# Performance work log

Hardware: AMD Instinct MI355X
Metric: run time of the kernel (lower is better)

## Reference

```python
import jax, jax.numpy as jnp
import numpy as np

N, D, H, E, K = 8192, 512, 2048, 8, 2  # tokens, input/output dim, hidden, experts, top-k
EPS = float(np.finfo(np.float64).eps)   # np.finfo(float).eps used by SparseDispatcher
NOISE_EPS = 1e-2                        # standard noisy-top-k gating epsilon


def setup_inputs() -> dict:
    key = jax.random.key(0)
    ks = jax.random.split(key, 8)
    s = 0.02  # weight scale to keep exp() in combine numerically sane
    return {
        "x": jax.random.normal(ks[0], (N, D), jnp.float32),
        "gate_feat": jax.random.normal(ks[1], (N, 2 * D), jnp.float32),
        "noise": jax.random.normal(ks[2], (N, E), jnp.float32),
        "w_gate": jax.random.normal(ks[3], (2 * D, E), jnp.float32) * s,
        "w_noise": jax.random.normal(ks[4], (2 * D, E), jnp.float32) * s,
        "fc1_w": jax.random.normal(ks[5], (E, H, D), jnp.float32) * s,
        "fc1_b": jnp.zeros((E, H), jnp.float32),
        "fc2_w": jax.random.normal(ks[6], (E, D, H), jnp.float32) * s,
        "fc2_b": jnp.zeros((E, D), jnp.float32),
    }


def reference(x, gate_feat, noise, w_gate, w_noise, fc1_w, fc1_b, fc2_w, fc2_b):
    # --- noisy top-k gating ---
    clean_logits = gate_feat @ w_gate                               # [N, E]
    noise_stddev = jax.nn.softplus(gate_feat @ w_noise) + NOISE_EPS  # [N, E]
    logits = clean_logits + noise * noise_stddev                    # randn_like * stddev
    top_vals, top_idx = jax.lax.top_k(logits, K + 1)                # top k+1 as in Shazeer gating
    top_k_gates = jax.nn.softmax(top_vals[:, :K], axis=-1)          # softmax over top-k logits
    gates = jnp.zeros_like(logits).at[jnp.arange(N)[:, None], top_idx[:, :K]].set(top_k_gates)

    # --- per-expert MLP (grouped GEMM; dense-masked form, math-equal to sparse dispatch
    # since zero-gate contributions vanish in the weighted combine) ---
    h = jax.nn.gelu(jnp.einsum('nd,ehd->enh', x, fc1_w) + fc1_b[:, None, :],
                    approximate=False)                              # torch nn.GELU = exact erf
    expert_out = jnp.einsum('enh,eoh->eno', h, fc2_w) + fc2_b[:, None, :]  # [E, N, D]

    # --- SparseDispatcher.combine: exp, gate-weight, scatter-add, eps-fill, log ---
    combined = jnp.einsum('ne,eno->no', gates, jnp.exp(expert_out))  # [N, D]
    combined = jnp.where(combined == 0, EPS, combined)
    return jnp.log(combined)
```

## Files before the change

### kernel.cpp

```cpp
#include <hip/hip_runtime.h>
#include <hip/hip_bf16.h>

#define NTOK 8192
#define DIM  512
#define HID  2048
#define NEXP 8
#define GFD  1024
#define NPAIR (NTOK*2)
#define EPSD 2.220446049250313e-16f
#define MAXTILES 136

typedef __bf16 bf16;
typedef __bf16 bf16x4 __attribute__((ext_vector_type(4)));
typedef __bf16 bf16x8 __attribute__((ext_vector_type(8)));
typedef float  f32x4  __attribute__((ext_vector_type(4)));

__device__ __forceinline__ void cvt4(const float* __restrict__ src,
                                     bf16* __restrict__ dst, int i) {
    float4 v = ((const float4*)src)[i];
    bf16x4 o = { (bf16)v.x, (bf16)v.y, (bf16)v.z, (bf16)v.w };
    ((bf16x4*)dst)[i] = o;
}

__global__ __launch_bounds__(256) void convert_kernel(
    const float* __restrict__ x, const float* __restrict__ w1,
    const float* __restrict__ w2,
    bf16* __restrict__ xo, bf16* __restrict__ w1o, bf16* __restrict__ w2o)
{
    int tid = blockIdx.x * 256 + threadIdx.x;
    int stride = gridDim.x * 256;
    for (int i = tid; i < NTOK*DIM/4; i += stride)      cvt4(x,  xo,  i);
    for (int i = tid; i < NEXP*HID*DIM/4; i += stride)  cvt4(w1, w1o, i);
    for (int i = tid; i < NEXP*DIM*HID/4; i += stride)  cvt4(w2, w2o, i);
}

__global__ __launch_bounds__(256) void gate_gemm_kernel(
    const float* __restrict__ gf, const float* __restrict__ wg,
    const float* __restrict__ wn, float* __restrict__ partial)
{
    const int bt = blockIdx.x;
    const int bd = blockIdx.y;
    const int tid = threadIdx.x;

    __shared__ float sgf[128*129];
    __shared__ float sw[128][16];

    #pragma unroll
    for (int i = 0; i < 4; ++i) {
        int idx = i*256 + tid;
        sw[idx>>3][idx&7]     = wg[bd*1024 + idx];
        sw[idx>>3][8+(idx&7)] = wn[bd*1024 + idx];
    }
    const float4* gf4 = (const float4*)gf;
    #pragma unroll
    for (int i = 0; i < 16; ++i) {
        int c = i*256 + tid;
        int row = c >> 5, c4 = c & 31;
        float4 v = gf4[(size_t)(bt*128+row)*(GFD/4) + bd*32 + c4];
        float* dst = sgf + row*129 + c4*4;
        dst[0]=v.x; dst[1]=v.y; dst[2]=v.z; dst[3]=v.w;
    }
    __syncthreads();

    const int og = tid >> 6;
    const int lane = tid & 63;
    const int t0 = lane*2, t1 = t0+1;
    float a0=0,a1=0,a2=0,a3=0, b0=0,b1=0,b2=0,b3=0;
    #pragma unroll 4
    for (int dd = 0; dd < 128; ++dd) {
        float f0 = sgf[t0*129+dd];
        float f1 = sgf[t1*129+dd];
        float4 w = *(const float4*)&sw[dd][og*4];
        a0 += f0*w.x; a1 += f0*w.y; a2 += f0*w.z; a3 += f0*w.w;
        b0 += f1*w.x; b1 += f1*w.y; b2 += f1*w.z; b3 += f1*w.w;
    }
    size_t pbase = ((size_t)bd*NTOK + bt*128)*16 + og*4;
    *(float4*)&partial[pbase + (size_t)t0*16] = make_float4(a0,a1,a2,a3);
    *(float4*)&partial[pbase + (size_t)t1*16] = make_float4(b0,b1,b2,b3);
}

__global__ __launch_bounds__(256) void finalize_kernel(
    const float* __restrict__ partial, const float* __restrict__ noise,
    int* __restrict__ tok_e, float* __restrict__ tok_g, int* __restrict__ counts)
{
    __shared__ int hist[8];
    int tid = threadIdx.x;
    if (tid < 8) hist[tid] = 0;
    __syncthreads();
    int n = blockIdx.x*256 + tid;

    float lg[16];
    #pragma unroll
    for (int k = 0; k < 16; ++k) lg[k] = 0.f;
    #pragma unroll
    for (int j = 0; j < 8; ++j) {
        const float4* p = (const float4*)(partial + ((size_t)j*NTOK + n)*16);
        float4 q0 = p[0], q1 = p[1], q2 = p[2], q3 = p[3];
        lg[0]+=q0.x; lg[1]+=q0.y; lg[2]+=q0.z; lg[3]+=q0.w;
        lg[4]+=q1.x; lg[5]+=q1.y; lg[6]+=q1.z; lg[7]+=q1.w;
        lg[8]+=q2.x; lg[9]+=q2.y; lg[10]+=q2.z; lg[11]+=q2.w;
        lg[12]+=q3.x; lg[13]+=q3.y; lg[14]+=q3.z; lg[15]+=q3.w;
    }
    float v0=-1e30f, v1=-1e30f; int i0=0, i1=0;
    #pragma unroll
    for (int e = 0; e < 8; ++e) {
        float xn = lg[8+e];
        float sp = fmaxf(xn, 0.f) + log1pf(expf(-fabsf(xn)));
        float l = lg[e] + noise[(size_t)n*NEXP+e] * (sp + 1e-2f);
        if (l > v0)      { v1=v0; i1=i0; v0=l; i0=e; }
        else if (l > v1) { v1=l; i1=e; }
    }
    float g1 = expf(v1 - v0);
    float s  = 1.0f + g1;
    tok_e[n] = i0 | (i1 << 8);
    tok_g[2*n]   = 1.0f / s;
    tok_g[2*n+1] = g1 / s;
    atomicAdd(&hist[i0], 1);
    atomicAdd(&hist[i1], 1);
    __syncthreads();
    if (tid < 8) atomicAdd(&counts[tid], hist[tid]);
}

__global__ void scan_kernel(const int* __restrict__ counts,
                            int* __restrict__ offsets, int* __restrict__ cursors,
                            int* __restrict__ tlist, int* __restrict__ ntiles)
{
    if (threadIdx.x == 0) {
        int s = 0, nt = 0;
        for (int e = 0; e < NEXP; ++e) {
            offsets[e] = s; cursors[e] = s;
            int c = counts[e];
            for (int mt = 0; mt*128 < c; ++mt) tlist[nt++] = e | (mt << 8);
            s += c;
        }
        offsets[NEXP] = s;
        ntiles[0] = nt;
    }
}

__global__ __launch_bounds__(256) void dispatch_kernel(
    const int* __restrict__ tok_e, const float* __restrict__ tok_g,
    int* __restrict__ cursors, int* __restrict__ pair_token, float* __restrict__ pair_gate,
    int* __restrict__ slot0, int* __restrict__ slot1)
{
    __shared__ int hist[8];
    __shared__ int base[8];
    int tid = threadIdx.x;
    if (tid < 8) hist[tid] = 0;
    __syncthreads();
    int n = blockIdx.x*256 + tid;
    int ee = tok_e[n];
    int e0 = ee & 255, e1 = (ee >> 8) & 255;
    atomicAdd(&hist[e0], 1);
    atomicAdd(&hist[e1], 1);
    __syncthreads();
    if (tid < 8) base[tid] = atomicAdd(&cursors[tid], hist[tid]);
    __syncthreads();
    int s0 = atomicAdd(&base[e0], 1);
    pair_token[s0] = n; pair_gate[s0] = tok_g[2*n];
    slot0[n] = s0;
    int s1 = atomicAdd(&base[e1], 1);
    pair_token[s1] = n; pair_gate[s1] = tok_g[2*n+1];
    slot1[n] = s1;
}

#define GLL16(gsrc, ldst) \
    __builtin_amdgcn_global_load_lds( \
        (__attribute__((address_space(1))) void*)(gsrc), \
        (__attribute__((address_space(3))) void*)(ldst), 16, 0, 0)

__global__ __launch_bounds__(512) void gemm1_kernel(
    const bf16* __restrict__ xb, const bf16* __restrict__ w1b,
    const float* __restrict__ fc1b,
    const int* __restrict__ pair_token, const int* __restrict__ offsets,
    const int* __restrict__ tlist, const int* __restrict__ ntiles,
    bf16* __restrict__ hbuf)
{
    const int ntp = blockIdx.x;
    const int tix = blockIdx.y;
    if (tix >= ntiles[0]) return;
    const int code = tlist[tix];
    const int e  = code & 255;
    const int mt = code >> 8;
    const int seg0 = offsets[e], seg1 = offsets[e+1];
    const int cnt = seg1 - seg0;
    const int mbase = mt * 128;

    __shared__ bf16 ldsA[128*64];
    __shared__ bf16 ldsB[256*64];

    const int tid = threadIdx.x;
    const int wid = tid >> 6;
    const int lane = tid & 63;
    const int wr = wid >> 2, wc = wid & 3;

    const bf16* srcA[2];
    const bf16* srcB[4];
    #pragma unroll
    for (int i = 0; i < 2; ++i) {
        int c = i*512 + tid;
        int r = c >> 3, c16 = c & 7;
        int sw = (c16 ^ (r & 7)) * 8;
        int p = seg0 + mbase + r;
        if (p > seg1 - 1) p = seg1 - 1;
        srcA[i] = xb + (size_t)pair_token[p] * DIM + sw;
    }
    #pragma unroll
    for (int i = 0; i < 4; ++i) {
        int c = i*512 + tid;
        int r = c >> 3, c16 = c & 7;
        int sw = (c16 ^ (r & 7)) * 8;
        srcB[i] = w1b + ((size_t)e*HID + ntp*256 + r) * DIM + sw;
    }

    f32x4 acc[4][4] = {};

    for (int kk = 0; kk < DIM; kk += 64) {
        #pragma unroll
        for (int i = 0; i < 2; ++i)
            GLL16(srcA[i] + kk, (char*)ldsA + i*8192 + tid*16);
        #pragma unroll
        for (int i = 0; i < 4; ++i)
            GLL16(srcB[i] + kk, (char*)ldsB + i*8192 + tid*16);
        __syncthreads();
        #pragma unroll
        for (int ks = 0; ks < 2; ++ks) {
            bf16x8 av[4], bv[4];
            #pragma unroll
            for (int m = 0; m < 4; ++m) {
                int row = wr*64 + m*16 + (lane & 15);
                int sw = (ks*4 + (lane >> 4)) ^ (row & 7);
                av[m] = *(const bf16x8*)(ldsA + row*64 + sw*8);
            }
            #pragma unroll
            for (int n = 0; n < 4; ++n) {
                int row = wc*64 + n*16 + (lane & 15);
                int sw = (ks*4 + (lane >> 4)) ^ (row & 7);
                bv[n] = *(const bf16x8*)(ldsB + row*64 + sw*8);
            }
            __builtin_amdgcn_s_setprio(1);
            #pragma unroll
            for (int m = 0; m < 4; ++m)
                #pragma unroll
                for (int n = 0; n < 4; ++n)
                    acc[m][n] = __builtin_amdgcn_mfma_f32_16x16x32_bf16(
                        av[m], bv[n], acc[m][n], 0, 0, 0);
            __builtin_amdgcn_s_setprio(0);
        }
        __syncthreads();
    }

    #pragma unroll
    for (int m = 0; m < 4; ++m) {
        #pragma unroll
        for (int jj = 0; jj < 4; ++jj) {
            int rt = wr*64 + m*16 + (lane >> 4)*4 + jj;
            int row = mbase + rt;
            if (row < cnt) {
                size_t hrow = (size_t)(seg0 + row) * HID;
                #pragma unroll
                for (int n = 0; n < 4; ++n) {
                    int col = ntp*256 + wc*64 + n*16 + (lane & 15);
                    float v = acc[m][n][jj] + fc1b[e*HID + col];
                    float g = 0.5f * v * (1.0f + erff(v * 0.70710678118654752f));
                    hbuf[hrow + col] = (bf16)g;
                }
            }
        }
    }
}

__global__ __launch_bounds__(256) void gemm2_kernel(
    const bf16* __restrict__ hbuf, const bf16* __restrict__ w2b,
    const float* __restrict__ fc2b,
    const float* __restrict__ pair_gate,
    const int* __restrict__ offsets,
    const int* __restrict__ tlist, const int* __restrict__ ntiles,
    bf16* __restrict__ pout)
{
    const int nt = blockIdx.x;
    const int tix = blockIdx.y;
    if (tix >= ntiles[0]) return;
    const int code = tlist[tix];
    const int e  = code & 255;
    const int mt = code >> 8;
    const int seg0 = offsets[e], seg1 = offsets[e+1];
    const int cnt = seg1 - seg0;
    const int mbase = mt * 128;

    __shared__ bf16 ldsA[128*64];
    __shared__ bf16 ldsB[128*64];

    const int tid = threadIdx.x;
    const int wid = tid >> 6;
    const int lane = tid & 63;
    const int wr = wid >> 1, wc = wid & 1;

    const bf16* srcA[4];
    const bf16* srcB[4];
    #pragma unroll
    for (int i = 0; i < 4; ++i) {
        int c = wid*256 + i*64 + lane;
        int r = c >> 3, c16 = c & 7;
        int sw = (c16 ^ (r & 7)) * 8;
        int p = seg0 + mbase + r;
        if (p > seg1 - 1) p = seg1 - 1;
        srcA[i] = hbuf + (size_t)p * HID + sw;
        srcB[i] = w2b + ((size_t)e*DIM + nt*128 + r) * HID + sw;
    }

    f32x4 acc[4][4] = {};

    for (int kk = 0; kk < HID; kk += 64) {
        #pragma unroll
        for (int i = 0; i < 4; ++i) {
            GLL16(srcA[i] + kk, (char*)ldsA + wid*4096 + i*1024);
            GLL16(srcB[i] + kk, (char*)ldsB + wid*4096 + i*1024);
        }
        __syncthreads();
        #pragma unroll
        for (int ks = 0; ks < 2; ++ks) {
            bf16x8 av[4], bv[4];
            #pragma unroll
            for (int m = 0; m < 4; ++m) {
                int row = wr*64 + m*16 + (lane & 15);
                int sw = (ks*4 + (lane >> 4)) ^ (row & 7);
                av[m] = *(const bf16x8*)(ldsA + row*64 + sw*8);
            }
            #pragma unroll
            for (int n = 0; n < 4; ++n) {
                int row = wc*64 + n*16 + (lane & 15);
                int sw = (ks*4 + (lane >> 4)) ^ (row & 7);
                bv[n] = *(const bf16x8*)(ldsB + row*64 + sw*8);
            }
            __builtin_amdgcn_s_setprio(1);
            #pragma unroll
            for (int m = 0; m < 4; ++m)
                #pragma unroll
                for (int n = 0; n < 4; ++n)
                    acc[m][n] = __builtin_amdgcn_mfma_f32_16x16x32_bf16(
                        av[m], bv[n], acc[m][n], 0, 0, 0);
            __builtin_amdgcn_s_setprio(0);
        }
        __syncthreads();
    }

    #pragma unroll
    for (int m = 0; m < 4; ++m) {
        #pragma unroll
        for (int jj = 0; jj < 4; ++jj) {
            int rt = wr*64 + m*16 + (lane >> 4)*4 + jj;
            int row = mbase + rt;
            if (row < cnt) {
                int p = seg0 + row;
                float gate = pair_gate[p];
                bf16* prow = pout + (size_t)p * DIM;
                #pragma unroll
                for (int n = 0; n < 4; ++n) {
                    int col = nt*128 + wc*64 + n*16 + (lane & 15);
                    float v = acc[m][n][jj] + fc2b[e*DIM + col];
                    prow[col] = (bf16)(gate * expf(v));
                }
            }
        }
    }
}

__global__ __launch_bounds__(256) void combine_kernel(
    const bf16* __restrict__ pout, const int* __restrict__ slot0,
    const int* __restrict__ slot1, float* __restrict__ out)
{
    const int wid = threadIdx.x >> 6;
    const int lane = threadIdx.x & 63;
    const int n = blockIdx.x*4 + wid;
    const int s0 = slot0[n], s1 = slot1[n];
    bf16x8 a = ((const bf16x8*)(pout + (size_t)s0 * DIM))[lane];
    bf16x8 b = ((const bf16x8*)(pout + (size_t)s1 * DIM))[lane];
    float4 r0, r1;
    float* orow = out + (size_t)n * DIM + lane*8;
    float c;
    c = (float)a[0] + (float)b[0]; r0.x = logf(c == 0.f ? EPSD : c);
    c = (float)a[1] + (float)b[1]; r0.y = logf(c == 0.f ? EPSD : c);
    c = (float)a[2] + (float)b[2]; r0.z = logf(c == 0.f ? EPSD : c);
    c = (float)a[3] + (float)b[3]; r0.w = logf(c == 0.f ? EPSD : c);
    c = (float)a[4] + (float)b[4]; r1.x = logf(c == 0.f ? EPSD : c);
    c = (float)a[5] + (float)b[5]; r1.y = logf(c == 0.f ? EPSD : c);
    c = (float)a[6] + (float)b[6]; r1.z = logf(c == 0.f ? EPSD : c);
    c = (float)a[7] + (float)b[7]; r1.w = logf(c == 0.f ? EPSD : c);
    ((float4*)orow)[0] = r0;
    ((float4*)orow)[1] = r1;
}

extern "C" void kernel_launch(void* const* d_in, const int* in_sizes, int n_in,
                              void* d_out, int out_size, void* d_ws, size_t ws_size,
                              hipStream_t stream)
{
    const float* x     = (const float*)d_in[0];
    const float* gf    = (const float*)d_in[1];
    const float* noise = (const float*)d_in[2];
    const float* wg    = (const float*)d_in[3];
    const float* wn    = (const float*)d_in[4];
    const float* fc1w  = (const float*)d_in[5];
    const float* fc1b  = (const float*)d_in[6];
    const float* fc2w  = (const float*)d_in[7];
    const float* fc2b  = (const float*)d_in[8];
    float* out = (float*)d_out;

    char* ws = (char*)d_ws;
    size_t off = 0;
    bf16* xb  = (bf16*)(ws + off); off += (size_t)NTOK*DIM*2;
    bf16* w1b = (bf16*)(ws + off); off += (size_t)NEXP*HID*DIM*2;
    bf16* w2b = (bf16*)(ws + off); off += (size_t)NEXP*DIM*HID*2;
    bf16* hb  = (bf16*)(ws + off); off += (size_t)NPAIR*HID*2;
    int*   pair_token = (int*)  (ws + off); off += (size_t)NPAIR*4;
    float* pair_gate  = (float*)(ws + off); off += (size_t)NPAIR*4;
    int*   tok_e      = (int*)  (ws + off); off += (size_t)NTOK*4;
    float* tok_g      = (float*)(ws + off); off += (size_t)NTOK*2*4;
    int*   slot0      = (int*)  (ws + off); off += (size_t)NTOK*4;
    int*   slot1      = (int*)  (ws + off); off += (size_t)NTOK*4;
    int*   counts     = (int*)  (ws + off); off += 64;
    int*   offsets    = (int*)  (ws + off); off += 64;
    int*   cursors    = (int*)  (ws + off); off += 64;
    int*   tlist      = (int*)  (ws + off); off += MAXTILES*4;
    int*   ntiles     = (int*)  (ws + off); off += 64;
    if (ws_size < off) return;

    float* partial = (float*)hb;
    bf16* pout = (bf16*)ws;

    hipMemsetAsync(counts, 0, 32, stream);
    convert_kernel<<<2048, 256, 0, stream>>>(x, fc1w, fc2w, xb, w1b, w2b);
    gate_gemm_kernel<<<dim3(64, 8), 256, 0, stream>>>(gf, wg, wn, partial);
    finalize_kernel<<<NTOK/256, 256, 0, stream>>>(partial, noise, tok_e, tok_g, counts);
    scan_kernel<<<1, 64, 0, stream>>>(counts, offsets, cursors, tlist, ntiles);
    dispatch_kernel<<<NTOK/256, 256, 0, stream>>>(tok_e, tok_g, cursors,
                                                  pair_token, pair_gate, slot0, slot1);
    gemm1_kernel<<<dim3(8, MAXTILES), 512, 0, stream>>>(xb, w1b, fc1b, pair_token, offsets,
                                                        tlist, ntiles, hb);
    gemm2_kernel<<<dim3(4, MAXTILES), 256, 0, stream>>>(hb, w2b, fc2b, pair_gate, offsets,
                                                        tlist, ntiles, pout);
    combine_kernel<<<NTOK/4, 256, 0, stream>>>(pout, slot0, slot1, out);
}
```

Baseline: 197.5 us.

## Double-buffer LDS tiles in both expert GEMMs to overlap loads with MFMA

Both grouped GEMM kernels now keep two LDS buffers per operand and issue the global-to-LDS loads for the next K-tile before computing on the current one. Partial vmcnt waits and raw s_barrier calls replace the full __syncthreads, so memory latency can hide behind MFMA work. This doubles LDS use per block, to 96KB in gemm1 and 64KB in gemm2, which may lower occupancy. It also relies on hand-counted vmcnt values matching the number of outstanding loads.

```diff
diff --git a/kernel.cpp b/kernel.cpp
--- a/kernel.cpp
+++ b/kernel.cpp
@@ -186,8 +186,8 @@
     const int cnt = seg1 - seg0;
     const int mbase = mt * 128;
 
-    __shared__ bf16 ldsA[128*64];
-    __shared__ bf16 ldsB[256*64];
+    __shared__ bf16 ldsA[2][128*64];
+    __shared__ bf16 ldsB[2][256*64];
 
     const int tid = threadIdx.x;
     const int wid = tid >> 6;
@@ -215,14 +215,27 @@
 
     f32x4 acc[4][4] = {};
 
-    for (int kk = 0; kk < DIM; kk += 64) {
-        #pragma unroll
-        for (int i = 0; i < 2; ++i)
-            GLL16(srcA[i] + kk, (char*)ldsA + i*8192 + tid*16);
-        #pragma unroll
-        for (int i = 0; i < 4; ++i)
-            GLL16(srcB[i] + kk, (char*)ldsB + i*8192 + tid*16);
-        __syncthreads();
+#define STAGE1(buf, kk) do { \
+    _Pragma("unroll") \
+    for (int i = 0; i < 2; ++i) \
+        GLL16(srcA[i] + (kk), (char*)ldsA[buf] + i*8192 + tid*16); \
+    _Pragma("unroll") \
+    for (int i = 0; i < 4; ++i) \
+        GLL16(srcB[i] + (kk), (char*)ldsB[buf] + i*8192 + tid*16); \
+    } while (0)
+
+    STAGE1(0, 0);
+
+    const int NT1 = DIM/64;
+    for (int t = 0; t < NT1; ++t) {
+        const int cur = t & 1;
+        if (t + 1 < NT1) {
+            STAGE1(1-cur, (t+1)*64);
+            asm volatile("s_waitcnt vmcnt(6)" ::: "memory");
+        } else {
+            asm volatile("s_waitcnt vmcnt(0)" ::: "memory");
+        }
+        __builtin_amdgcn_s_barrier();
         #pragma unroll
         for (int ks = 0; ks < 2; ++ks) {
             bf16x8 av[4], bv[4];
@@ -230,13 +243,13 @@
             for (int m = 0; m < 4; ++m) {
                 int row = wr*64 + m*16 + (lane & 15);
                 int sw = (ks*4 + (lane >> 4)) ^ (row & 7);
-                av[m] = *(const bf16x8*)(ldsA + row*64 + sw*8);
+                av[m] = *(const bf16x8*)(ldsA[cur] + row*64 + sw*8);
             }
             #pragma unroll
             for (int n = 0; n < 4; ++n) {
                 int row = wc*64 + n*16 + (lane & 15);
                 int sw = (ks*4 + (lane >> 4)) ^ (row & 7);
-                bv[n] = *(const bf16x8*)(ldsB + row*64 + sw*8);
+                bv[n] = *(const bf16x8*)(ldsB[cur] + row*64 + sw*8);
             }
             __builtin_amdgcn_s_setprio(1);
             #pragma unroll
@@ -247,7 +260,7 @@
                         av[m], bv[n], acc[m][n], 0, 0, 0);
             __builtin_amdgcn_s_setprio(0);
         }
-        __syncthreads();
+        __builtin_amdgcn_s_barrier();
     }
 
     #pragma unroll
@@ -288,8 +301,8 @@
     const int cnt = seg1 - seg0;
     const int mbase = mt * 128;
 
-    __shared__ bf16 ldsA[128*64];
-    __shared__ bf16 ldsB[128*64];
+    __shared__ bf16 ldsA[2][128*64];
+    __shared__ bf16 ldsB[2][128*64];
 
     const int tid = threadIdx.x;
     const int wid = tid >> 6;
@@ -311,13 +324,25 @@
 
     f32x4 acc[4][4] = {};
 
-    for (int kk = 0; kk < HID; kk += 64) {
-        #pragma unroll
-        for (int i = 0; i < 4; ++i) {
-            GLL16(srcA[i] + kk, (char*)ldsA + wid*4096 + i*1024);
-            GLL16(srcB[i] + kk, (char*)ldsB + wid*4096 + i*1024);
-        }
-        __syncthreads();
+#define STAGE2(buf, kk) do { \
+    _Pragma("unroll") \
+    for (int i = 0; i < 4; ++i) { \
+        GLL16(srcA[i] + (kk), (char*)ldsA[buf] + wid*4096 + i*1024); \
+        GLL16(srcB[i] + (kk), (char*)ldsB[buf] + wid*4096 + i*1024); \
+    } } while (0)
+
+    STAGE2(0, 0);
+
+    const int NT2 = HID/64;
+    for (int t = 0; t < NT2; ++t) {
+        const int cur = t & 1;
+        if (t + 1 < NT2) {
+            STAGE2(1-cur, (t+1)*64);
+            asm volatile("s_waitcnt vmcnt(8)" ::: "memory");
+        } else {
+            asm volatile("s_waitcnt vmcnt(0)" ::: "memory");
+        }
+        __builtin_amdgcn_s_barrier();
         #pragma unroll
         for (int ks = 0; ks < 2; ++ks) {
             bf16x8 av[4], bv[4];
@@ -325,13 +350,13 @@
             for (int m = 0; m < 4; ++m) {
                 int row = wr*64 + m*16 + (lane & 15);
                 int sw = (ks*4 + (lane >> 4)) ^ (row & 7);
-                av[m] = *(const bf16x8*)(ldsA + row*64 + sw*8);
+                av[m] = *(const bf16x8*)(ldsA[cur] + row*64 + sw*8);
             }
             #pragma unroll
             for (int n = 0; n < 4; ++n) {
                 int row = wc*64 + n*16 + (lane & 15);
                 int sw = (ks*4 + (lane >> 4)) ^ (row & 7);
-                bv[n] = *(const bf16x8*)(ldsB + row*64 + sw*8);
+                bv[n] = *(const bf16x8*)(ldsB[cur] + row*64 + sw*8);
             }
             __builtin_amdgcn_s_setprio(1);
             #pragma unroll
@@ -342,7 +367,7 @@
                         av[m], bv[n], acc[m][n], 0, 0, 0);
             __builtin_amdgcn_s_setprio(0);
         }
-        __syncthreads();
+        __builtin_amdgcn_s_barrier();
     }
 
     #pragma unroll
```

New measurement: 242.7 us. +22.8%, slower.

## Double-buffer gemm2 LDS tiles with K=32 stages to overlap loads and MFMA

Applied to the files above, without the earlier changes.

Splits the second grouped GEMM's K loop into 32-wide stages held in two LDS buffers. The next stage's global-to-LDS loads are issued before computing on the current one, using a partial vmcnt wait, so memory latency overlaps the MFMAs. The LDS swizzle is adjusted for the 32-wide rows. The cost is twice as many barriers per unit of K and less MFMA work per barrier.

```diff
diff --git a/kernel.cpp b/kernel.cpp
--- a/kernel.cpp
+++ b/kernel.cpp
@@ -288,21 +288,21 @@
     const int cnt = seg1 - seg0;
     const int mbase = mt * 128;
 
-    __shared__ bf16 ldsA[128*64];
-    __shared__ bf16 ldsB[128*64];
+    __shared__ bf16 ldsA[2][128*32];
+    __shared__ bf16 ldsB[2][128*32];
 
     const int tid = threadIdx.x;
     const int wid = tid >> 6;
     const int lane = tid & 63;
     const int wr = wid >> 1, wc = wid & 1;
 
-    const bf16* srcA[4];
-    const bf16* srcB[4];
-    #pragma unroll
-    for (int i = 0; i < 4; ++i) {
-        int c = wid*256 + i*64 + lane;
-        int r = c >> 3, c16 = c & 7;
-        int sw = (c16 ^ (r & 7)) * 8;
+    const bf16* srcA[2];
+    const bf16* srcB[2];
+    #pragma unroll
+    for (int i = 0; i < 2; ++i) {
+        int c = i*256 + tid;
+        int r = c >> 2, s = c & 3;
+        int sw = (s ^ ((r >> 1) & 3)) * 8;
         int p = seg0 + mbase + r;
         if (p > seg1 - 1) p = seg1 - 1;
         srcA[i] = hbuf + (size_t)p * HID + sw;
@@ -311,27 +311,38 @@
 
     f32x4 acc[4][4] = {};
 
-    for (int kk = 0; kk < HID; kk += 64) {
-        #pragma unroll
-        for (int i = 0; i < 4; ++i) {
-            GLL16(srcA[i] + kk, (char*)ldsA + wid*4096 + i*1024);
-            GLL16(srcB[i] + kk, (char*)ldsB + wid*4096 + i*1024);
-        }
-        __syncthreads();
-        #pragma unroll
-        for (int ks = 0; ks < 2; ++ks) {
+#define STAGE2(buf, kk) do { \
+    _Pragma("unroll") \
+    for (int i = 0; i < 2; ++i) { \
+        GLL16(srcA[i] + (kk), (char*)ldsA[buf] + i*4096 + tid*16); \
+        GLL16(srcB[i] + (kk), (char*)ldsB[buf] + i*4096 + tid*16); \
+    } } while (0)
+
+    STAGE2(0, 0);
+
+    const int NT2 = HID/32;
+    for (int t = 0; t < NT2; ++t) {
+        const int cur = t & 1;
+        if (t + 1 < NT2) {
+            STAGE2(1-cur, (t+1)*32);
+            asm volatile("s_waitcnt vmcnt(4)" ::: "memory");
+        } else {
+            asm volatile("s_waitcnt vmcnt(0)" ::: "memory");
+        }
+        __builtin_amdgcn_s_barrier();
+        {
             bf16x8 av[4], bv[4];
             #pragma unroll
             for (int m = 0; m < 4; ++m) {
                 int row = wr*64 + m*16 + (lane & 15);
-                int sw = (ks*4 + (lane >> 4)) ^ (row & 7);
-                av[m] = *(const bf16x8*)(ldsA + row*64 + sw*8);
+                int sw = (lane >> 4) ^ ((row >> 1) & 3);
+                av[m] = *(const bf16x8*)(ldsA[cur] + row*32 + sw*8);
             }
             #pragma unroll
             for (int n = 0; n < 4; ++n) {
                 int row = wc*64 + n*16 + (lane & 15);
-                int sw = (ks*4 + (lane >> 4)) ^ (row & 7);
-                bv[n] = *(const bf16x8*)(ldsB + row*64 + sw*8);
+                int sw = (lane >> 4) ^ ((row >> 1) & 3);
+                bv[n] = *(const bf16x8*)(ldsB[cur] + row*32 + sw*8);
             }
             __builtin_amdgcn_s_setprio(1);
             #pragma unroll
@@ -342,7 +353,7 @@
                         av[m], bv[n], acc[m][n], 0, 0, 0);
             __builtin_amdgcn_s_setprio(0);
         }
-        __syncthreads();
+        __builtin_amdgcn_s_barrier();
     }
 
     #pragma unroll
```

Result: slower. 209.8 us (+6.2%).
